# Kernel optimization log

Hardware: AMD Instinct MI355X
Metric: run time of the kernel (lower is better)

Reference implementation:

```python
import jax, jax.numpy as jnp
import numpy as np

T, B, I, H, O, K = 512, 64, 128, 512, 128, 32


def setup_inputs() -> dict:
    key = jax.random.key(0)
    ks = jax.random.split(key, 7)
    sc = 1.0 / np.sqrt(I + H)
    return {
        "inputs": jax.random.normal(ks[0], (T, B, I), jnp.float32),
        "W_i": jax.random.normal(ks[1], (I + H, H), jnp.float32) * sc,
        "b_i": jnp.zeros((H,), jnp.float32),
        "W_o": jax.random.normal(ks[2], (I + H, H), jnp.float32) * sc,
        "b_o": jnp.zeros((H,), jnp.float32),
        "W_c": jax.random.normal(ks[3], (I + H, H), jnp.float32) * sc,
        "b_c": jnp.zeros((H,), jnp.float32),
        "W_out": jax.random.normal(ks[4], (H, O), jnp.float32) * (1.0 / np.sqrt(H)),
        "b_out": jnp.zeros((O,), jnp.float32),
        "d_values": jax.random.normal(ks[5], (1, H), jnp.float32) * 0.1,
    }


def _get_wd(d, k):
    # d: [1,H] fractional orders in (0, 0.5).
    # Fractional differencing weights of (1-L)^d: v_0=1, v_{i+1}=v_i*(i-d)/(i+1).
    # Returned weights_d[j] = v_{k-j} (oldest lag first), matching get_w/get_wd.
    dv = d[0]  # [H]

    def step(v, i):
        v_next = v * (i - dv) / (i + 1.0)
        return v_next, v_next

    _, vs = jax.lax.scan(step, jnp.ones_like(dv), jnp.arange(k, dtype=d.dtype))
    return vs[::-1]  # [K, H] = [v_k, ..., v_1]


def reference(inputs, W_i, b_i, W_o, b_o, W_c, b_c, W_out, b_out, d_values):
    d = 0.5 * jax.nn.sigmoid(d_values)          # [1,H]
    wd = _get_wd(d, K)                           # [K,H]
    Tn, Bn, _ = inputs.shape
    Hn = W_i.shape[1]
    h0 = jnp.zeros((Bn, Hn), inputs.dtype)
    hc0 = jnp.zeros((K, Bn, Hn), inputs.dtype)   # lagged cell states, oldest first

    def step(carry, x_t):
        h, hc = carry
        z = jnp.concatenate([x_t, h], axis=1)    # [B, I+H]
        i = jax.nn.sigmoid(z @ W_i + b_i)
        o = jax.nn.sigmoid(z @ W_o + b_o)
        g = jnp.tanh(z @ W_c + b_c)
        # fractional-differencing memory: c_t = i*g - sum_j v_j c_{t-j}
        c = i * g - jnp.einsum("kh,kbh->bh", wd, hc)
        h_new = o * jnp.tanh(c)
        hc_new = jnp.concatenate([hc[1:], c[None]], axis=0)
        out = h_new @ W_out + b_out
        return (h_new, hc_new), out

    (h_last, hc_last), outputs = jax.lax.scan(step, (h0, hc0), inputs)
    return outputs, h_last, hc_last
```

## Files before the change

### kernel.cpp

```cpp
#include <hip/hip_runtime.h>
#include <hip/hip_bf16.h>

#define TT 512
#define BB 64
#define II 128
#define HH 512
#define OO 128
#define KLAG 32
#define GWG 32
#define HC 16
#define KKX 4
#define KKT 20

typedef __attribute__((ext_vector_type(8))) short short8;
typedef __attribute__((ext_vector_type(4))) int   i32x4;
typedef __attribute__((ext_vector_type(4))) float f32x4;
typedef unsigned short u16;

__device__ __forceinline__ float sigmoidf_(float x){ return 1.f/(1.f+__expf(-x)); }
__device__ __forceinline__ float tanhf_(float x){ float e = __expf(2.f*x); return 1.f - 2.f/(e+1.f); }
__device__ __forceinline__ u16 f2bf(float f){
  __hip_bfloat16 h = __float2bfloat16(f);
  u16 u; __builtin_memcpy(&u, &h, 2); return u;
}

__device__ __forceinline__ short8 ld_sc_b128(const u16* p){
  i32x4 r;
  asm volatile("global_load_dwordx4 %0, %1, off sc0 sc1" : "=v"(r) : "v"(p));
  return __builtin_bit_cast(short8, r);
}
__device__ __forceinline__ void st_sc_b16(u16* p, unsigned int v){
  asm volatile("global_store_short %0, %1, off sc0 sc1" :: "v"(p), "v"(v) : "memory");
}

__global__ void k_cast_x(const float* __restrict__ x, u16* __restrict__ xb, int n4){
  int i = blockIdx.x*256 + threadIdx.x;
  if (i >= n4) return;
  float4 v = ((const float4*)x)[i];
  ushort4 o;
  o.x = f2bf(v.x); o.y = f2bf(v.y); o.z = f2bf(v.z); o.w = f2bf(v.w);
  ((ushort4*)xb)[i] = o;
}

__global__ void k_pack_w(const float* __restrict__ Wi, const float* __restrict__ Wo,
                         const float* __restrict__ Wc, u16* __restrict__ wp){
  int idx = blockIdx.x*256 + threadIdx.x;
  int j    = idx & 7;
  int lane = (idx >> 3) & 63;
  int kk   = (idx >> 9) % KKT;
  int rest = (idx >> 9) / KKT;
  int gate = rest % 3;
  int gh   = rest / 3;
  int k    = kk*32 + ((lane>>4)<<3) + j;
  int col  = gh*HC + (lane & 15);
  const float* W = (gate==0) ? Wi : ((gate==1) ? Wo : Wc);
  wp[idx] = f2bf(W[(size_t)k*HH + col]);
}

__global__ void k_pack_wo(const float* __restrict__ Wout, u16* __restrict__ wp){
  int idx = blockIdx.x*256 + threadIdx.x;
  int j    = idx & 7;
  int lane = (idx >> 3) & 63;
  int kk   = (idx >> 9) & 15;
  int nt   = idx >> 13;
  int k    = kk*32 + ((lane>>4)<<3) + j;
  int col  = nt*16 + (lane & 15);
  wp[idx] = f2bf(Wout[(size_t)k*OO + col]);
}

__global__ void k_zero(unsigned int* __restrict__ h0_u32, int n, int* __restrict__ flags){
  int i = blockIdx.x*256 + threadIdx.x;
  if (i < n) h0_u32[i] = 0;
  if (blockIdx.x == 0){
    for (int f = threadIdx.x; f < GWG*16; f += 256) flags[f] = 0;
  }
}

__global__ __launch_bounds__(256, 1) void k_recur(
    const u16* __restrict__ xb,
    const u16* __restrict__ wp,
    const float* __restrict__ bi_p, const float* __restrict__ bo_p,
    const float* __restrict__ bc_p, const float* __restrict__ dv,
    u16* __restrict__ hsq,
    float* __restrict__ hlast,
    float* __restrict__ hclast,
    int* __restrict__ flags)
{
  const int gh  = blockIdx.x;
  const int tid = threadIdx.x;
  const int w = tid >> 6, l = tid & 63, lg = l >> 4, lr = l & 15;
  const int ch = gh*HC + lr;

  float d = 0.5f * sigmoidf_(dv[ch]);
  float v[KLAG];
  float vc = 1.f;
  #pragma unroll
  for (int j = 0; j < KLAG; ++j){ vc *= ((float)j - d)/((float)(j+1)); v[j] = vc; }
  const float bi = bi_p[ch], bo = bo_p[ch], bc = bc_p[ch];

  float hist[4][KLAG];
  #pragma unroll
  for (int r = 0; r < 4; ++r){
    #pragma unroll
    for (int q = 0; q < KLAG; ++q) hist[r][q] = 0.f;
  }

  const u16* wbase = wp + (size_t)gh*(3*KKT*64*8);
  const int arow  = w*16 + lr;
  const int browb = w*16 + lg*4;

  for (int t = 0; t < TT; ++t){
    float fs[4];
    #pragma unroll
    for (int r = 0; r < 4; ++r){
      float s = 0.f;
      #pragma unroll
      for (int q = 0; q < KLAG; ++q) s = __builtin_fmaf(v[q], hist[r][q], s);
      fs[r] = s;
    }
    f32x4 acc0 = {0.f,0.f,0.f,0.f};
    f32x4 acc1 = {0.f,0.f,0.f,0.f};
    f32x4 acc2 = {0.f,0.f,0.f,0.f};
    const u16* xrow = xb + ((size_t)t*BB + arow)*II + lg*8;
    #pragma unroll
    for (int kk = 0; kk < KKX; ++kk){
      short8 a = *(const short8*)(xrow + kk*32);
      const u16* wk = wbase + (size_t)kk*(64*8) + l*8;
      short8 b0 = *(const short8*)(wk);
      short8 b1 = *(const short8*)(wk + (size_t)1*KKT*64*8);
      short8 b2 = *(const short8*)(wk + (size_t)2*KKT*64*8);
      acc0 = __builtin_amdgcn_mfma_f32_16x16x32_bf16(a, b0, acc0, 0,0,0);
      acc1 = __builtin_amdgcn_mfma_f32_16x16x32_bf16(a, b1, acc1, 0,0,0);
      acc2 = __builtin_amdgcn_mfma_f32_16x16x32_bf16(a, b2, acc2, 0,0,0);
    }

    if (tid < GWG){
      while (__hip_atomic_load(flags + tid*16, __ATOMIC_RELAXED, __HIP_MEMORY_SCOPE_AGENT) < t){ }
    }
    __syncthreads();

    const u16* hrow = hsq + (size_t)t*(BB*HH) + (size_t)arow*HH + lg*8;
    short8 ha[16];
    #pragma unroll
    for (int kk = 0; kk < 16; ++kk) ha[kk] = ld_sc_b128(hrow + kk*32);
    asm volatile("s_waitcnt vmcnt(0)" ::: "memory");
    __builtin_amdgcn_sched_barrier(0);
    #pragma unroll
    for (int kk = 0; kk < 16; ++kk){
      const u16* wk = wbase + (size_t)(kk+KKX)*(64*8) + l*8;
      short8 b0 = *(const short8*)(wk);
      short8 b1 = *(const short8*)(wk + (size_t)1*KKT*64*8);
      short8 b2 = *(const short8*)(wk + (size_t)2*KKT*64*8);
      acc0 = __builtin_amdgcn_mfma_f32_16x16x32_bf16(ha[kk], b0, acc0, 0,0,0);
      acc1 = __builtin_amdgcn_mfma_f32_16x16x32_bf16(ha[kk], b1, acc1, 0,0,0);
      acc2 = __builtin_amdgcn_mfma_f32_16x16x32_bf16(ha[kk], b2, acc2, 0,0,0);
    }

    u16* hdst = hsq + (size_t)(t+1)*(BB*HH);
    #pragma unroll
    for (int r = 0; r < 4; ++r){
      float ig = sigmoidf_(acc0[r] + bi);
      float og = sigmoidf_(acc1[r] + bo);
      float gg = tanhf_(acc2[r] + bc);
      float c = ig*gg - fs[r];
      #pragma unroll
      for (int q = KLAG-1; q > 0; --q) hist[r][q] = hist[r][q-1];
      hist[r][0] = c;
      float h = og * tanhf_(c);
      int row = browb + r;
      st_sc_b16(hdst + (size_t)row*HH + ch, (unsigned int)f2bf(h));
      if (t == TT-1) hlast[(size_t)row*HH + ch] = h;
    }
    asm volatile("s_waitcnt vmcnt(0)" ::: "memory");
    __syncthreads();
    if (tid == 0){
      __hip_atomic_store(flags + gh*16, t+1, __ATOMIC_RELEASE, __HIP_MEMORY_SCOPE_AGENT);
    }
  }

  #pragma unroll
  for (int r = 0; r < 4; ++r){
    int row = browb + r;
    #pragma unroll
    for (int q = 0; q < KLAG; ++q){
      hclast[(size_t)(KLAG-1-q)*(BB*HH) + (size_t)row*HH + ch] = hist[r][q];
    }
  }
}

__global__ __launch_bounds__(256) void k_out(
    const u16* __restrict__ hseq, const u16* __restrict__ wop,
    const float* __restrict__ b_out, float* __restrict__ out)
{
  const int tid = threadIdx.x, w = tid>>6, l = tid&63, lg = l>>4, lr = l&15;
  const size_t rbase = (size_t)blockIdx.x*64 + (size_t)w*16;
  f32x4 acc[8];
  #pragma unroll
  for (int n = 0; n < 8; ++n) acc[n] = (f32x4){0.f,0.f,0.f,0.f};
  const u16* arow_p = hseq + (rbase + lr)*HH + lg*8;
  #pragma unroll
  for (int kk = 0; kk < 16; ++kk){
    short8 a = *(const short8*)(arow_p + kk*32);
    #pragma unroll
    for (int n = 0; n < 8; ++n){
      short8 b = *(const short8*)(wop + ((size_t)(n*16 + kk)*64 + l)*8);
      acc[n] = __builtin_amdgcn_mfma_f32_16x16x32_bf16(a, b, acc[n], 0,0,0);
    }
  }
  #pragma unroll
  for (int n = 0; n < 8; ++n){
    int col = n*16 + lr;
    float bb = b_out[col];
    #pragma unroll
    for (int r = 0; r < 4; ++r)
      out[(rbase + lg*4 + r)*OO + col] = acc[n][r] + bb;
  }
}

extern "C" void kernel_launch(void* const* d_in, const int* in_sizes, int n_in,
                              void* d_out, int out_size, void* d_ws, size_t ws_size,
                              hipStream_t stream){
  const float* x    = (const float*)d_in[0];
  const float* Wi   = (const float*)d_in[1];
  const float* bi   = (const float*)d_in[2];
  const float* Wo   = (const float*)d_in[3];
  const float* bo   = (const float*)d_in[4];
  const float* Wc   = (const float*)d_in[5];
  const float* bc   = (const float*)d_in[6];
  const float* Wout = (const float*)d_in[7];
  const float* bout = (const float*)d_in[8];
  const float* dv   = (const float*)d_in[9];

  char* ws = (char*)d_ws;
  u16* xb    = (u16*)(ws);
  u16* wp    = (u16*)(ws + 8388608);
  u16* wop   = (u16*)(ws + 10354688);
  u16* hsq   = (u16*)(ws + 10485760);
  int* flags = (int*)(ws + 44105728);

  float* outp   = (float*)d_out;
  float* hlast  = outp + (size_t)TT*BB*OO;
  float* hclast = hlast + (size_t)BB*HH;

  hipLaunchKernelGGL(k_cast_x, dim3(4096), dim3(256), 0, stream, x, xb, TT*BB*II/4);
  hipLaunchKernelGGL(k_pack_w, dim3(3840), dim3(256), 0, stream, Wi, Wo, Wc, wp);
  hipLaunchKernelGGL(k_pack_wo, dim3(256), dim3(256), 0, stream, Wout, wop);
  hipLaunchKernelGGL(k_zero, dim3(64), dim3(256), 0, stream, (unsigned int*)hsq, (BB*HH*2)/4, flags);
  hipLaunchKernelGGL(k_recur, dim3(GWG), dim3(256), 0, stream,
                     xb, wp, bi, bo, bc, dv, hsq, hlast, hclast, flags);
  hipLaunchKernelGGL(k_out, dim3(512), dim3(256), 0, stream, hsq + (size_t)BB*HH, wop, bout, outp);
}
```

Baseline: 3.380 ms.

## Run redundant recurrence groups per XCD with L2-local sync and LDS weights

Launches 256 workgroups that register per XCD through an atomic roster. The first 32 on each XCD form an independent replica of the recurrence and synchronise through per-XCD flags using L2-scoped (sc0) loads and stores instead of system-coherent ones. The first replica to finish sets a done flag, and the others bail out of their spin loops. Recurrent-weight tiles are also cached in LDS and the input-weight fragments in registers, which removes repeated global weight loads each step. The risks are that replicas race to write the same hsq buffer, and that correctness relies on cross-XCD write visibility for the output kernel.

New measurement: 2.888 ms. -14.6%, faster.

```diff
diff --git a/kernel.cpp b/kernel.cpp
--- a/kernel.cpp
+++ b/kernel.cpp
@@ -11,6 +11,7 @@
 #define HC 16
 #define KKX 4
 #define KKT 20
+#define NXCD 8
 
 typedef __attribute__((ext_vector_type(8))) short short8;
 typedef __attribute__((ext_vector_type(4))) int   i32x4;
@@ -22,15 +23,6 @@
 __device__ __forceinline__ u16 f2bf(float f){
   __hip_bfloat16 h = __float2bfloat16(f);
   u16 u; __builtin_memcpy(&u, &h, 2); return u;
-}
-
-__device__ __forceinline__ short8 ld_sc_b128(const u16* p){
-  i32x4 r;
-  asm volatile("global_load_dwordx4 %0, %1, off sc0 sc1" : "=v"(r) : "v"(p));
-  return __builtin_bit_cast(short8, r);
-}
-__device__ __forceinline__ void st_sc_b16(u16* p, unsigned int v){
-  asm volatile("global_store_short %0, %1, off sc0 sc1" :: "v"(p), "v"(v) : "memory");
 }
 
 __global__ void k_cast_x(const float* __restrict__ x, u16* __restrict__ xb, int n4){
@@ -68,12 +60,10 @@
   wp[idx] = f2bf(Wout[(size_t)k*OO + col]);
 }
 
-__global__ void k_zero(unsigned int* __restrict__ h0_u32, int n, int* __restrict__ flags){
+__global__ void k_zero(unsigned int* __restrict__ h0, unsigned int* __restrict__ misc){
   int i = blockIdx.x*256 + threadIdx.x;
-  if (i < n) h0_u32[i] = 0;
-  if (blockIdx.x == 0){
-    for (int f = threadIdx.x; f < GWG*16; f += 256) flags[f] = 0;
-  }
+  if (i < 16384) h0[i] = 0;
+  else if (i < 16384 + 4240) misc[i - 16384] = 0;
 }
 
 __global__ __launch_bounds__(256, 1) void k_recur(
@@ -84,13 +74,45 @@
     u16* __restrict__ hsq,
     float* __restrict__ hlast,
     float* __restrict__ hclast,
-    int* __restrict__ flags)
+    int* flags,
+    int* rost,
+    int* done)
 {
-  const int gh  = blockIdx.x;
+  __shared__ u16 wlds[3*16*64*8];
+  __shared__ int sslot, sxcd, sbail;
   const int tid = threadIdx.x;
+  if (tid == 0){
+    unsigned int xcd;
+    asm volatile("s_getreg_b32 %0, hwreg(HW_REG_XCC_ID)" : "=s"(xcd));
+    sxcd  = (int)(xcd & 7);
+    sslot = __hip_atomic_fetch_add(rost + (xcd & 7)*16, 1,
+                                   __ATOMIC_RELAXED, __HIP_MEMORY_SCOPE_AGENT);
+    sbail = 0;
+  }
+  __syncthreads();
+  const int gh = sslot, xcd = sxcd;
+  if (gh >= GWG) return;
+
+  __builtin_amdgcn_fence(__ATOMIC_ACQUIRE, "agent");
+
+  const u16* wbase = wp + (size_t)gh*(3*KKT*64*8);
+  for (int i = tid*8; i < 3*16*64*8; i += 256*8){
+    int e = i & 511;
+    int blk = i >> 9;
+    int g = blk >> 4, kkh = blk & 15;
+    *(short8*)&wlds[i] = *(const short8*)(wbase + (size_t)(g*KKT + KKX + kkh)*512 + e);
+  }
   const int w = tid >> 6, l = tid & 63, lg = l >> 4, lr = l & 15;
+  short8 bx[KKX][3];
+  #pragma unroll
+  for (int kk = 0; kk < KKX; ++kk){
+    #pragma unroll
+    for (int g = 0; g < 3; ++g)
+      bx[kk][g] = *(const short8*)(wbase + (size_t)(g*KKT + kk)*512 + l*8);
+  }
+  __syncthreads();
+
   const int ch = gh*HC + lr;
-
   float d = 0.5f * sigmoidf_(dv[ch]);
   float v[KLAG];
   float vc = 1.f;
@@ -105,11 +127,14 @@
     for (int q = 0; q < KLAG; ++q) hist[r][q] = 0.f;
   }
 
-  const u16* wbase = wp + (size_t)gh*(3*KKT*64*8);
   const int arow  = w*16 + lr;
   const int browb = w*16 + lg*4;
+  int* fme = flags + (xcd*GWG + gh)*16;
+  bool bailed = false;
 
   for (int t = 0; t < TT; ++t){
+    u16* hdst = hsq + (size_t)(t+1)*(BB*HH);
+
     float fs[4];
     #pragma unroll
     for (int r = 0; r < 4; ++r){
@@ -125,38 +150,50 @@
     #pragma unroll
     for (int kk = 0; kk < KKX; ++kk){
       short8 a = *(const short8*)(xrow + kk*32);
-      const u16* wk = wbase + (size_t)kk*(64*8) + l*8;
-      short8 b0 = *(const short8*)(wk);
-      short8 b1 = *(const short8*)(wk + (size_t)1*KKT*64*8);
-      short8 b2 = *(const short8*)(wk + (size_t)2*KKT*64*8);
-      acc0 = __builtin_amdgcn_mfma_f32_16x16x32_bf16(a, b0, acc0, 0,0,0);
-      acc1 = __builtin_amdgcn_mfma_f32_16x16x32_bf16(a, b1, acc1, 0,0,0);
-      acc2 = __builtin_amdgcn_mfma_f32_16x16x32_bf16(a, b2, acc2, 0,0,0);
+      acc0 = __builtin_amdgcn_mfma_f32_16x16x32_bf16(a, bx[kk][0], acc0, 0,0,0);
+      acc1 = __builtin_amdgcn_mfma_f32_16x16x32_bf16(a, bx[kk][1], acc1, 0,0,0);
+      acc2 = __builtin_amdgcn_mfma_f32_16x16x32_bf16(a, bx[kk][2], acc2, 0,0,0);
     }
 
     if (tid < GWG){
-      while (__hip_atomic_load(flags + tid*16, __ATOMIC_RELAXED, __HIP_MEMORY_SCOPE_AGENT) < t){ }
+      const int* fp = flags + (xcd*GWG + tid)*16;
+      int it = 0;
+      while (true){
+        int fv;
+        asm volatile("global_load_dword %0, %1, off sc0\ns_waitcnt vmcnt(0)"
+                     : "=v"(fv) : "v"(fp));
+        if (fv >= t) break;
+        if (((++it) & 63) == 0){
+          int dn;
+          asm volatile("global_load_dword %0, %1, off sc0 sc1\ns_waitcnt vmcnt(0)"
+                       : "=v"(dn) : "v"(done));
+          if (dn){ sbail = 1; break; }
+        }
+      }
     }
     __syncthreads();
+    if (sbail){ bailed = true; break; }
 
     const u16* hrow = hsq + (size_t)t*(BB*HH) + (size_t)arow*HH + lg*8;
     short8 ha[16];
     #pragma unroll
-    for (int kk = 0; kk < 16; ++kk) ha[kk] = ld_sc_b128(hrow + kk*32);
+    for (int kk = 0; kk < 16; ++kk){
+      i32x4 r;
+      asm volatile("global_load_dwordx4 %0, %1, off sc0" : "=v"(r) : "v"(hrow + kk*32));
+      ha[kk] = __builtin_bit_cast(short8, r);
+    }
     asm volatile("s_waitcnt vmcnt(0)" ::: "memory");
     __builtin_amdgcn_sched_barrier(0);
     #pragma unroll
     for (int kk = 0; kk < 16; ++kk){
-      const u16* wk = wbase + (size_t)(kk+KKX)*(64*8) + l*8;
-      short8 b0 = *(const short8*)(wk);
-      short8 b1 = *(const short8*)(wk + (size_t)1*KKT*64*8);
-      short8 b2 = *(const short8*)(wk + (size_t)2*KKT*64*8);
+      short8 b0 = *(const short8*)&wlds[(size_t)((0*16 + kk)*64 + l)*8];
+      short8 b1 = *(const short8*)&wlds[(size_t)((1*16 + kk)*64 + l)*8];
+      short8 b2 = *(const short8*)&wlds[(size_t)((2*16 + kk)*64 + l)*8];
       acc0 = __builtin_amdgcn_mfma_f32_16x16x32_bf16(ha[kk], b0, acc0, 0,0,0);
       acc1 = __builtin_amdgcn_mfma_f32_16x16x32_bf16(ha[kk], b1, acc1, 0,0,0);
       acc2 = __builtin_amdgcn_mfma_f32_16x16x32_bf16(ha[kk], b2, acc2, 0,0,0);
     }
 
-    u16* hdst = hsq + (size_t)(t+1)*(BB*HH);
     #pragma unroll
     for (int r = 0; r < 4; ++r){
       float ig = sigmoidf_(acc0[r] + bi);
@@ -168,22 +205,30 @@
       hist[r][0] = c;
       float h = og * tanhf_(c);
       int row = browb + r;
-      st_sc_b16(hdst + (size_t)row*HH + ch, (unsigned int)f2bf(h));
+      unsigned int hb = (unsigned int)f2bf(h);
+      u16* sp = hdst + (size_t)row*HH + ch;
+      asm volatile("global_store_short %0, %1, off sc0" :: "v"(sp), "v"(hb) : "memory");
       if (t == TT-1) hlast[(size_t)row*HH + ch] = h;
     }
     asm volatile("s_waitcnt vmcnt(0)" ::: "memory");
     __syncthreads();
     if (tid == 0){
-      __hip_atomic_store(flags + gh*16, t+1, __ATOMIC_RELEASE, __HIP_MEMORY_SCOPE_AGENT);
-    }
-  }
-
-  #pragma unroll
-  for (int r = 0; r < 4; ++r){
-    int row = browb + r;
-    #pragma unroll
-    for (int q = 0; q < KLAG; ++q){
-      hclast[(size_t)(KLAG-1-q)*(BB*HH) + (size_t)row*HH + ch] = hist[r][q];
+      int val = t+1;
+      asm volatile("global_store_dword %0, %1, off sc0" :: "v"(fme), "v"(val) : "memory");
+    }
+  }
+
+  if (!bailed){
+    #pragma unroll
+    for (int r = 0; r < 4; ++r){
+      int row = browb + r;
+      #pragma unroll
+      for (int q = 0; q < KLAG; ++q)
+        hclast[(size_t)(KLAG-1-q)*(BB*HH) + (size_t)row*HH + ch] = hist[r][q];
+    }
+    if (tid == 0){
+      int one = 1;
+      asm volatile("global_store_dword %0, %1, off sc0 sc1" :: "v"(done), "v"(one) : "memory");
     }
   }
 }
@@ -237,6 +282,8 @@
   u16* wop   = (u16*)(ws + 10354688);
   u16* hsq   = (u16*)(ws + 10485760);
   int* flags = (int*)(ws + 44105728);
+  int* rost  = (int*)(ws + 44122112);
+  int* done  = (int*)(ws + 44122624);
 
   float* outp   = (float*)d_out;
   float* hlast  = outp + (size_t)TT*BB*OO;
@@ -245,8 +292,9 @@
   hipLaunchKernelGGL(k_cast_x, dim3(4096), dim3(256), 0, stream, x, xb, TT*BB*II/4);
   hipLaunchKernelGGL(k_pack_w, dim3(3840), dim3(256), 0, stream, Wi, Wo, Wc, wp);
   hipLaunchKernelGGL(k_pack_wo, dim3(256), dim3(256), 0, stream, Wout, wop);
-  hipLaunchKernelGGL(k_zero, dim3(64), dim3(256), 0, stream, (unsigned int*)hsq, (BB*HH*2)/4, flags);
-  hipLaunchKernelGGL(k_recur, dim3(GWG), dim3(256), 0, stream,
-                     xb, wp, bi, bo, bc, dv, hsq, hlast, hclast, flags);
+  hipLaunchKernelGGL(k_zero, dim3(81), dim3(256), 0, stream,
+                     (unsigned int*)hsq, (unsigned int*)flags);
+  hipLaunchKernelGGL(k_recur, dim3(256), dim3(256), 0, stream,
+                     xb, wp, bi, bo, bc, dv, hsq, hlast, hclast, flags, rost, done);
   hipLaunchKernelGGL(k_out, dim3(512), dim3(256), 0, stream, hsq + (size_t)BB*HH, wop, bout, outp);
 }
```
